# Optimization experiments

Hardware: AMD Instinct MI355X
Metric: run time of the kernel (lower is better)

The kernel has to match this reference:

```python
import jax, jax.numpy as jnp
import numpy as np

B, S, D_MODEL, H = 4, 1024, 1024, 16
HD = D_MODEL // H  # head_dim = 64


def setup_inputs() -> dict:
    key = jax.random.key(0)
    ks = jax.random.split(key, 12)
    sd = 1.0 / np.sqrt(D_MODEL)
    return {
        "x": jax.random.normal(ks[0], (B, S, D_MODEL), dtype=jnp.float32),
        "Wq": jax.random.normal(ks[1], (D_MODEL, D_MODEL), dtype=jnp.float32) * sd,
        "bq": jnp.zeros((D_MODEL,), dtype=jnp.float32),
        "Wk": jax.random.normal(ks[2], (D_MODEL, D_MODEL), dtype=jnp.float32) * sd,
        "bk": jnp.zeros((D_MODEL,), dtype=jnp.float32),
        "Wv": jax.random.normal(ks[3], (D_MODEL, D_MODEL), dtype=jnp.float32) * sd,
        "bv": jnp.zeros((D_MODEL,), dtype=jnp.float32),
        "W1": jax.random.normal(ks[4], (2 * D_MODEL, D_MODEL), dtype=jnp.float32) * sd,
        "b1": jnp.zeros((2 * D_MODEL,), dtype=jnp.float32),
        "W2": jax.random.normal(ks[5], (D_MODEL, 2 * D_MODEL), dtype=jnp.float32) * (1.0 / np.sqrt(2 * D_MODEL)),
        "b2": jnp.zeros((D_MODEL,), dtype=jnp.float32),
        "mask": jnp.ones((B, S, S), dtype=jnp.int32),
    }


def reference(x, Wq, bq, Wk, bk, Wv, bv, W1, b1, W2, b2, mask):
    # QKV projections (torch Linear: y = x @ W.T + b), split into heads -> [B,H,S,HD]
    def proj(W, b):
        return (x @ W.T + b).reshape(B, S, H, HD).transpose(0, 2, 1, 3)

    q = proj(Wq, bq)
    k = proj(Wk, bk)
    v = proj(Wv, bv)

    scores = jnp.einsum("bhqd,bhkd->bhqk", q, k) / jnp.sqrt(jnp.float32(HD))
    # mask [B,S,S] broadcast over heads (original does unsqueeze(1).repeat)
    scores = jnp.where(mask[:, None, :, :] == 0, jnp.float32(-1e8), scores)
    probs = jax.nn.softmax(scores, axis=-1)
    ctx = jnp.einsum("bhqk,bhkd->bhqd", probs, v)
    ctx = ctx.transpose(0, 2, 1, 3).reshape(B, S, D_MODEL)

    # out-projection MLP: Linear(d, 2d) -> ReLU -> Linear(2d, d)
    h = jax.nn.relu(ctx @ W1.T + b1)
    return h @ W2.T + b2
```

## Files before the change

kernel.cpp:

```cpp
#include <hip/hip_runtime.h>
#include <hip/hip_bf16.h>
#include <stdint.h>


#define B_ 4
#define S_ 1024
#define DM_ 1024
#define H_ 16
#define HD_ 64

typedef __attribute__((ext_vector_type(8))) short short8;
typedef __attribute__((ext_vector_type(4))) float f32x4;
typedef __attribute__((ext_vector_type(4))) unsigned short ushort4v;

#define GLB_AS(p) ((const __attribute__((address_space(1))) void*)(p))
#define LDS_AS(p) ((__attribute__((address_space(3))) void*)(p))

__device__ __forceinline__ void async_load16(const void* g, void* l) {
  __builtin_amdgcn_global_load_lds(GLB_AS(g), LDS_AS(l), 16, 0, 0);
}

__device__ __forceinline__ unsigned short f2bf(float x) {
  union { float f; unsigned int u; } v; v.f = x;
  unsigned int r = v.u + 0x7fffu + ((v.u >> 16) & 1u);
  return (unsigned short)(r >> 16);
}

#define QSCALE 0.18033688011112042f

struct ConvArgs {
  const float* src[6];
  unsigned short* dst[6];
  int n4[6];
};

__global__ void convert_bf16_kernel(ConvArgs a) {
  const int seg = blockIdx.y;
  const int n4 = a.n4[seg];
  const f32x4* __restrict__ src = (const f32x4*)a.src[seg];
  ushort4v* __restrict__ dst = (ushort4v*)a.dst[seg];
  for (int i = blockIdx.x * blockDim.x + threadIdx.x; i < n4;
       i += gridDim.x * blockDim.x) {
    f32x4 v = src[i];
    ushort4v o;
    o[0] = f2bf(v[0]); o[1] = f2bf(v[1]); o[2] = f2bf(v[2]); o[3] = f2bf(v[3]);
    dst[i] = o;
  }
}

__global__ void pack_mask_kernel(const int* __restrict__ mask,
                                 unsigned long long* __restrict__ bits,
                                 unsigned int* __restrict__ rowflag) {
  const int row = blockIdx.x * 4 + (threadIdx.x >> 6);
  const int lane = threadIdx.x & 63;
  const int* mr = mask + (size_t)row * S_;
  unsigned long long allf = ~0ull;
#pragma unroll
  for (int g = 0; g < 16; ++g) {
    int mv = mr[g * 64 + lane];
    unsigned long long bal = __ballot(mv != 0);
    if (lane == g) bits[(size_t)row * 16 + g] = bal;
    allf &= bal;
  }
  if (lane == 0) rowflag[row] = (allf == ~0ull) ? 1u : 0u;
}

__global__ void concat_bias_kernel(const float* __restrict__ bq,
                                   const float* __restrict__ bk,
                                   const float* __restrict__ bv,
                                   float* __restrict__ cb) {
  int i = blockIdx.x * 256 + threadIdx.x;
  const float* src = (i < 1024) ? bq : (i < 2048) ? bk : bv;
  cb[i] = src[i & 1023];
}

enum { EPI_QKV = 0, EPI_RELU_BF16 = 2, EPI_F32 = 3, EPI_PARTIAL = 4 };

template <int EPI>
__global__ __launch_bounds__(256, 3) void gemm_bt(
    const unsigned short* __restrict__ A, const unsigned short* __restrict__ Bt,
    const float* __restrict__ bias, void* __restrict__ Cp, int M, int N, int K,
    int Kld) {
  __shared__ unsigned short sA[128 * 32];
  __shared__ unsigned short sB[128 * 32];

  const int tid = threadIdx.x;
  const int lane = tid & 63;
  const int wave = tid >> 6;
  const int quad = lane >> 4;
  const int l15 = lane & 15;
  const int m0 = blockIdx.y * 128;
  const int n0 = blockIdx.x * 128;
  const int wm = (wave >> 1) * 64;
  const int wn = (wave & 1) * 64;
  const int kz = blockIdx.z * K;

  f32x4 acc[4][4];
#pragma unroll
  for (int i = 0; i < 4; ++i)
#pragma unroll
    for (int j = 0; j < 4; ++j) acc[i][j] = (f32x4){0.f, 0.f, 0.f, 0.f};

  const int srow = tid >> 2;
  const int scol = (tid & 3) * 8;
  const unsigned short* gA = A + (size_t)(m0 + srow) * Kld + kz + scol;
  const unsigned short* gB = Bt + (size_t)(n0 + srow) * Kld + kz + scol;
  unsigned short* lA = sA + tid * 8;
  unsigned short* lB = sB + tid * 8;

  for (int k0 = 0; k0 < K; k0 += 32) {
    __syncthreads();
    async_load16(gA + k0, lA);
    async_load16(gA + (size_t)64 * Kld + k0, lA + 64 * 32);
    async_load16(gB + k0, lB);
    async_load16(gB + (size_t)64 * Kld + k0, lB + 64 * 32);
    __syncthreads();

    short8 af[4], bfr[4];
#pragma unroll
    for (int t = 0; t < 4; ++t) {
      af[t] = *(const short8*)(sA + (wm + t * 16 + l15) * 32 + quad * 8);
      bfr[t] = *(const short8*)(sB + (wn + t * 16 + l15) * 32 + quad * 8);
    }
#pragma unroll
    for (int mt = 0; mt < 4; ++mt)
#pragma unroll
      for (int nt = 0; nt < 4; ++nt)
        acc[mt][nt] = __builtin_amdgcn_mfma_f32_16x16x32_bf16(
            af[mt], bfr[nt], acc[mt][nt], 0, 0, 0);
  }

#pragma unroll
  for (int nt = 0; nt < 4; ++nt) {
    const int col = n0 + wn + nt * 16 + l15;
    const float bv = (EPI == EPI_PARTIAL) ? 0.f : bias[col];
#pragma unroll
    for (int mt = 0; mt < 4; ++mt) {
#pragma unroll
      for (int r = 0; r < 4; ++r) {
        const int row = m0 + wm + mt * 16 + quad * 4 + r;
        float v = acc[mt][nt][r] + bv;
        if (EPI == EPI_F32) {
          ((float*)Cp)[(size_t)row * N + col] = v;
        } else if (EPI == EPI_PARTIAL) {
          ((float*)Cp)[(size_t)blockIdx.z * M * N + (size_t)row * N + col] = v;
        } else if (EPI == EPI_RELU_BF16) {
          ((unsigned short*)Cp)[(size_t)row * N + col] = f2bf(fmaxf(v, 0.f));
        } else {
          const int proj = col >> 10;
          const int c = col & 1023;
          const int hh = c >> 6, dd = c & 63;
          const int bb = row >> 10, ss = row & 1023;
          size_t off = (size_t)proj * (B_ * H_ * S_ * HD_) +
                       (size_t)(bb * 16 + hh) * (S_ * HD_);
          if (proj == 2)
            off += (size_t)dd * S_ + ss;
          else
            off += (size_t)ss * HD_ + dd;
          const float scl = (proj == 0) ? QSCALE : 1.0f;
          ((unsigned short*)Cp)[off] = f2bf(v * scl);
        }
      }
    }
  }
}

__global__ __launch_bounds__(256, 2) void flash_attn(
    const unsigned short* __restrict__ Q, const unsigned short* __restrict__ Kh,
    const unsigned short* __restrict__ Vt,
    const unsigned long long* __restrict__ mbits,
    const unsigned int* __restrict__ mrowflag,
    unsigned short* __restrict__ ctx) {
  __shared__ unsigned short sK[128 * 64];
  __shared__ unsigned short sV[64 * 128];
  __shared__ unsigned short spb[4][32 * 136];

  const int tid = threadIdx.x;
  const int wave = tid >> 6;
  const int lane = tid & 63;
  const int quad = lane >> 4;
  const int l15 = lane & 15;
  const int bh = blockIdx.x;
  const int b = bh >> 4;
  const int h = bh & 15;
  const int qbase = blockIdx.y * 128 + wave * 32;

  const unsigned short* Qb = Q + (size_t)bh * S_ * HD_;
  const unsigned short* Kb = Kh + (size_t)bh * S_ * HD_;
  const unsigned short* Vb = Vt + (size_t)bh * HD_ * S_;
  unsigned short* pbuf = spb[wave];

  bool mask_all_ones;
  {
    unsigned int f = mrowflag[b * S_ + qbase + (lane & 31)];
    mask_all_ones = (__ballot(f != 0) == ~0ull);
  }

  short8 qf[2][2];
#pragma unroll
  for (int u = 0; u < 2; ++u)
#pragma unroll
    for (int ks = 0; ks < 2; ++ks)
      qf[u][ks] = *(const short8*)(Qb + (size_t)(qbase + u * 16 + l15) * HD_ +
                                   ks * 32 + quad * 8);

  f32x4 o[2][4];
#pragma unroll
  for (int u = 0; u < 2; ++u)
#pragma unroll
    for (int i = 0; i < 4; ++i) o[u][i] = (f32x4){0.f, 0.f, 0.f, 0.f};
  float lsum[2][4] = {{0.f, 0.f, 0.f, 0.f}, {0.f, 0.f, 0.f, 0.f}};

  for (int kt = 0; kt < S_ / 128; ++kt) {
    const int kbase = kt * 128;

    __syncthreads();
#pragma unroll
    for (int st = 0; st < 4; ++st) {
      const int j = st * 256 + tid;
      const int r = j >> 3, c = j & 7;
      async_load16(Kb + (size_t)(kbase + r) * HD_ + ((c ^ (r & 7)) * 8),
                   sK + j * 8);
    }
#pragma unroll
    for (int st = 0; st < 4; ++st) {
      const int j = st * 256 + tid;
      const int d = j >> 4, c = j & 15;
      async_load16(Vb + (size_t)d * S_ + kbase + ((c ^ (d & 15)) * 8),
                   sV + j * 8);
    }
    __syncthreads();

    f32x4 s[2][8];
#pragma unroll
    for (int u = 0; u < 2; ++u)
#pragma unroll
      for (int i = 0; i < 8; ++i) s[u][i] = (f32x4){0.f, 0.f, 0.f, 0.f};
#pragma unroll
    for (int ks = 0; ks < 2; ++ks) {
      const int cg = ks * 4 + quad;
#pragma unroll
      for (int nt = 0; nt < 8; ++nt) {
        const int row = nt * 16 + l15;
        const short8 kf =
            *(const short8*)(sK + row * 64 + ((cg ^ (row & 7)) * 8));
        s[0][nt] = __builtin_amdgcn_mfma_f32_16x16x32_bf16(qf[0][ks], kf,
                                                           s[0][nt], 0, 0, 0);
        s[1][nt] = __builtin_amdgcn_mfma_f32_16x16x32_bf16(qf[1][ks], kf,
                                                           s[1][nt], 0, 0, 0);
      }
    }

    if (!mask_all_ones) {
#pragma unroll
      for (int u = 0; u < 2; ++u)
#pragma unroll
        for (int r = 0; r < 4; ++r) {
          const int q = qbase + u * 16 + quad * 4 + r;
          const unsigned long long* wp =
              mbits + ((size_t)(b * S_ + q)) * 16 + kt * 2;
          const unsigned long long w0 = wp[0], w1 = wp[1];
#pragma unroll
          for (int nt = 0; nt < 8; ++nt) {
            const unsigned long long w = (nt < 4) ? w0 : w1;
            const int bit = (nt * 16 + l15) & 63;
            if (!((w >> bit) & 1)) s[u][nt][r] = -1.0e8f;
          }
        }
    }

#pragma unroll
    for (int u = 0; u < 2; ++u)
#pragma unroll
      for (int nt = 0; nt < 8; ++nt)
#pragma unroll
        for (int r = 0; r < 4; ++r) {
          const float p = __builtin_amdgcn_exp2f(s[u][nt][r]);
          lsum[u][r] += p;
          pbuf[(u * 16 + quad * 4 + r) * 136 + nt * 16 + l15] = f2bf(p);
        }

#pragma unroll
    for (int ks2 = 0; ks2 < 4; ++ks2) {
      const short8 pf0 =
          *(const short8*)(pbuf + l15 * 136 + ks2 * 32 + quad * 8);
      const short8 pf1 =
          *(const short8*)(pbuf + (16 + l15) * 136 + ks2 * 32 + quad * 8);
      const int cg = ks2 * 4 + quad;
#pragma unroll
      for (int nt = 0; nt < 4; ++nt) {
        const int d = nt * 16 + l15;
        const short8 vf =
            *(const short8*)(sV + d * 128 + ((cg ^ (d & 15)) * 8));
        o[0][nt] = __builtin_amdgcn_mfma_f32_16x16x32_bf16(pf0, vf, o[0][nt], 0, 0, 0);
        o[1][nt] = __builtin_amdgcn_mfma_f32_16x16x32_bf16(pf1, vf, o[1][nt], 0, 0, 0);
      }
    }
  }

#pragma unroll
  for (int u = 0; u < 2; ++u)
#pragma unroll
    for (int r = 0; r < 4; ++r) {
      float lr = lsum[u][r];
      lr += __shfl_xor(lr, 1);
      lr += __shfl_xor(lr, 2);
      lr += __shfl_xor(lr, 4);
      lr += __shfl_xor(lr, 8);
      const float inv = 1.0f / lr;
#pragma unroll
      for (int nt = 0; nt < 4; ++nt)
        pbuf[(u * 16 + quad * 4 + r) * 68 + nt * 16 + l15] =
            f2bf(o[u][nt][r] * inv);
    }
#pragma unroll
  for (int i = 0; i < 4; ++i) {
    const int j = i * 64 + lane;
    const int r = j >> 3, c = j & 7;
    const short8 val = *(const short8*)(pbuf + r * 68 + c * 8);
    *(short8*)(ctx + ((size_t)b * S_ + qbase + r) * DM_ + h * HD_ + c * 8) = val;
  }
}

__global__ void reduce_ffn2_kernel(const float* __restrict__ part,
                                   const float* __restrict__ b2,
                                   float* __restrict__ out) {
  const int i = blockIdx.x * 256 + threadIdx.x;
  const f32x4 a = ((const f32x4*)part)[i];
  const f32x4 b = ((const f32x4*)part)[i + (B_ * S_ * DM_ / 4)];
  const f32x4 bb = ((const f32x4*)b2)[i & 255];
  ((f32x4*)out)[i] = a + b + bb;
}

extern "C" void kernel_launch(void* const* d_in, const int* in_sizes, int n_in,
                              void* d_out, int out_size, void* d_ws,
                              size_t ws_size, hipStream_t stream) {
  const float* x = (const float*)d_in[0];
  const float* Wq = (const float*)d_in[1];
  const float* bq = (const float*)d_in[2];
  const float* Wk = (const float*)d_in[3];
  const float* bk = (const float*)d_in[4];
  const float* Wv = (const float*)d_in[5];
  const float* bv = (const float*)d_in[6];
  const float* W1 = (const float*)d_in[7];
  const float* b1 = (const float*)d_in[8];
  const float* W2 = (const float*)d_in[9];
  const float* b2 = (const float*)d_in[10];
  const int* mask = (const int*)d_in[11];
  float* out = (float*)d_out;

  char* ws = (char*)d_ws;
  unsigned short* xb   = (unsigned short*)(ws + 0);
  unsigned short* wqkv = (unsigned short*)(ws + 8388608);
  unsigned short* w1b  = (unsigned short*)(ws + 14680064);
  unsigned short* w2b  = (unsigned short*)(ws + 18874368);
  unsigned short* QKVh = (unsigned short*)(ws + 23068672);
  unsigned short* ctxb = (unsigned short*)(ws + 48234496);
  unsigned short* hb   = (unsigned short*)(ws + 56623104);
  unsigned long long* mbits = (unsigned long long*)(ws + 73400320);
  unsigned int* mrowflag    = (unsigned int*)(ws + 73924608);
  float* cb                 = (float*)(ws + 73940992);
  float* part = (float*)(ws + 23068672);

  ConvArgs ca;
  ca.src[0] = x;  ca.dst[0] = xb;               ca.n4[0] = (B_ * S_ * DM_) / 4;
  ca.src[1] = Wq; ca.dst[1] = wqkv;             ca.n4[1] = (DM_ * DM_) / 4;
  ca.src[2] = Wk; ca.dst[2] = wqkv + DM_ * DM_; ca.n4[2] = (DM_ * DM_) / 4;
  ca.src[3] = Wv; ca.dst[3] = wqkv + 2 * DM_ * DM_; ca.n4[3] = (DM_ * DM_) / 4;
  ca.src[4] = W1; ca.dst[4] = w1b;              ca.n4[4] = (2 * DM_ * DM_) / 4;
  ca.src[5] = W2; ca.dst[5] = w2b;              ca.n4[5] = (2 * DM_ * DM_) / 4;
  convert_bf16_kernel<<<dim3(256, 6), 256, 0, stream>>>(ca);

  pack_mask_kernel<<<dim3((B_ * S_) / 4), 256, 0, stream>>>(mask, mbits, mrowflag);
  concat_bias_kernel<<<dim3(12), 256, 0, stream>>>(bq, bk, bv, cb);

  const int M = B_ * S_;
  gemm_bt<EPI_QKV><<<dim3(3 * DM_ / 128, M / 128), 256, 0, stream>>>(
      xb, wqkv, cb, QKVh, M, 3 * DM_, DM_, DM_);

  flash_attn<<<dim3(B_ * H_, S_ / 128), 256, 0, stream>>>(
      QKVh, QKVh + B_ * H_ * S_ * HD_, QKVh + 2 * B_ * H_ * S_ * HD_,
      mbits, mrowflag, ctxb);

  gemm_bt<EPI_RELU_BF16><<<dim3((2 * DM_) / 128, M / 128), 256, 0, stream>>>(
      ctxb, w1b, b1, hb, M, 2 * DM_, DM_, DM_);

  gemm_bt<EPI_PARTIAL><<<dim3(DM_ / 128, M / 128, 2), 256, 0, stream>>>(
      hb, w2b, b2, part, M, DM_, DM_, 2 * DM_);
  reduce_ffn2_kernel<<<dim3(M * DM_ / 4 / 256), 256, 0, stream>>>(part, b2, out);
}
```

Measured before the change: 258.7 us.

## Deepen GEMM K-tile to 64 with XOR swizzle; store QKV row-major and transpose V separately

The GEMM K tile doubles from 32 to 64 and the LDS layout gets an XOR swizzle, which halves the number of barrier pairs per K loop and should avoid LDS bank conflicts. The QKV GEMM now writes a plain row-major [M,3072] bf16 output instead of the scattered head-split and transposed-V stores, so its epilogue writes are coalesced. A new transpose_v kernel builds V^T (stored in the now-free xb region), and flash_attn reads Q and K with a 3072 row stride. The trade-offs are one more kernel launch, an extra pass over V, strided Q/K loads in attention, and more LDS per GEMM block, which may lower occupancy.

Result: faster. 246.1 us (-4.9%).

```diff
diff --git a/kernel.cpp b/kernel.cpp
--- a/kernel.cpp
+++ b/kernel.cpp
@@ -81,14 +81,15 @@
     const unsigned short* __restrict__ A, const unsigned short* __restrict__ Bt,
     const float* __restrict__ bias, void* __restrict__ Cp, int M, int N, int K,
     int Kld) {
-  __shared__ unsigned short sA[128 * 32];
-  __shared__ unsigned short sB[128 * 32];
+  __shared__ unsigned short sA[128 * 64];
+  __shared__ unsigned short sB[128 * 64];
 
   const int tid = threadIdx.x;
   const int lane = tid & 63;
   const int wave = tid >> 6;
   const int quad = lane >> 4;
   const int l15 = lane & 15;
+  const int swzb = l15 & 7;
   const int m0 = blockIdx.y * 128;
   const int n0 = blockIdx.x * 128;
   const int wm = (wave >> 1) * 64;
@@ -101,39 +102,45 @@
 #pragma unroll
     for (int j = 0; j < 4; ++j) acc[i][j] = (f32x4){0.f, 0.f, 0.f, 0.f};
 
-  const int srow = tid >> 2;
-  const int scol = (tid & 3) * 8;
+  const int srow = tid >> 3;
+  const int scol = ((tid & 7) ^ (srow & 7)) * 8;
   const unsigned short* gA = A + (size_t)(m0 + srow) * Kld + kz + scol;
   const unsigned short* gB = Bt + (size_t)(n0 + srow) * Kld + kz + scol;
   unsigned short* lA = sA + tid * 8;
   unsigned short* lB = sB + tid * 8;
 
-  for (int k0 = 0; k0 < K; k0 += 32) {
+  for (int k0 = 0; k0 < K; k0 += 64) {
     __syncthreads();
-    async_load16(gA + k0, lA);
-    async_load16(gA + (size_t)64 * Kld + k0, lA + 64 * 32);
-    async_load16(gB + k0, lB);
-    async_load16(gB + (size_t)64 * Kld + k0, lB + 64 * 32);
+#pragma unroll
+    for (int st = 0; st < 4; ++st) {
+      async_load16(gA + (size_t)(st * 32) * Kld + k0, lA + st * 2048);
+      async_load16(gB + (size_t)(st * 32) * Kld + k0, lB + st * 2048);
+    }
     __syncthreads();
 
-    short8 af[4], bfr[4];
-#pragma unroll
-    for (int t = 0; t < 4; ++t) {
-      af[t] = *(const short8*)(sA + (wm + t * 16 + l15) * 32 + quad * 8);
-      bfr[t] = *(const short8*)(sB + (wn + t * 16 + l15) * 32 + quad * 8);
-    }
-#pragma unroll
-    for (int mt = 0; mt < 4; ++mt)
-#pragma unroll
-      for (int nt = 0; nt < 4; ++nt)
-        acc[mt][nt] = __builtin_amdgcn_mfma_f32_16x16x32_bf16(
-            af[mt], bfr[nt], acc[mt][nt], 0, 0, 0);
+#pragma unroll
+    for (int ks = 0; ks < 2; ++ks) {
+      short8 af[4], bfr[4];
+#pragma unroll
+      for (int t = 0; t < 4; ++t) {
+        const int cg = ((ks * 4 + quad) ^ swzb) * 8;
+        af[t] = *(const short8*)(sA + (wm + t * 16 + l15) * 64 + cg);
+        bfr[t] = *(const short8*)(sB + (wn + t * 16 + l15) * 64 + cg);
+      }
+#pragma unroll
+      for (int mt = 0; mt < 4; ++mt)
+#pragma unroll
+        for (int nt = 0; nt < 4; ++nt)
+          acc[mt][nt] = __builtin_amdgcn_mfma_f32_16x16x32_bf16(
+              af[mt], bfr[nt], acc[mt][nt], 0, 0, 0);
+    }
   }
 
 #pragma unroll
   for (int nt = 0; nt < 4; ++nt) {
     const int col = n0 + wn + nt * 16 + l15;
     const float bv = (EPI == EPI_PARTIAL) ? 0.f : bias[col];
+    const float scl = (EPI == EPI_QKV && col < 1024) ? QSCALE : 1.0f;
 #pragma unroll
     for (int mt = 0; mt < 4; ++mt) {
 #pragma unroll
@@ -147,27 +154,45 @@
         } else if (EPI == EPI_RELU_BF16) {
           ((unsigned short*)Cp)[(size_t)row * N + col] = f2bf(fmaxf(v, 0.f));
         } else {
-          const int proj = col >> 10;
-          const int c = col & 1023;
-          const int hh = c >> 6, dd = c & 63;
-          const int bb = row >> 10, ss = row & 1023;
-          size_t off = (size_t)proj * (B_ * H_ * S_ * HD_) +
-                       (size_t)(bb * 16 + hh) * (S_ * HD_);
-          if (proj == 2)
-            off += (size_t)dd * S_ + ss;
-          else
-            off += (size_t)ss * HD_ + dd;
-          const float scl = (proj == 0) ? QSCALE : 1.0f;
-          ((unsigned short*)Cp)[off] = f2bf(v * scl);
+          ((unsigned short*)Cp)[(size_t)row * N + col] = f2bf(v * scl);
         }
       }
     }
   }
 }
 
+__global__ __launch_bounds__(256) void transpose_v(
+    const unsigned short* __restrict__ Cqkv, unsigned short* __restrict__ Vt) {
+  __shared__ unsigned short t[128 * 65];
+  const int bh = blockIdx.x;
+  const int stile = blockIdx.y;
+  const int b = bh >> 4, h = bh & 15;
+  const int tid = threadIdx.x;
+  const unsigned short* src =
+      Cqkv + ((size_t)(b * S_) + stile * 128) * 3072 + 2048 + h * 64;
+#pragma unroll
+  for (int ps = 0; ps < 4; ++ps) {
+    const int idx = ps * 256 + tid;
+    const int r = idx >> 3, c = idx & 7;
+    const short8 v = *(const short8*)(src + (size_t)r * 3072 + c * 8);
+#pragma unroll
+    for (int i = 0; i < 8; ++i) t[r * 65 + c * 8 + i] = (unsigned short)v[i];
+  }
+  __syncthreads();
+  unsigned short* dst = Vt + (size_t)bh * HD_ * S_ + stile * 128;
+#pragma unroll
+  for (int ps = 0; ps < 4; ++ps) {
+    const int idx = ps * 256 + tid;
+    const int d = idx >> 4, sc = idx & 15;
+    short8 v;
+#pragma unroll
+    for (int i = 0; i < 8; ++i) v[i] = (short)t[(sc * 8 + i) * 65 + d];
+    *(short8*)(dst + (size_t)d * S_ + sc * 8) = v;
+  }
+}
+
 __global__ __launch_bounds__(256, 2) void flash_attn(
-    const unsigned short* __restrict__ Q, const unsigned short* __restrict__ Kh,
-    const unsigned short* __restrict__ Vt,
+    const unsigned short* __restrict__ Cqkv, const unsigned short* __restrict__ Vt,
     const unsigned long long* __restrict__ mbits,
     const unsigned int* __restrict__ mrowflag,
     unsigned short* __restrict__ ctx) {
@@ -185,8 +210,8 @@
   const int h = bh & 15;
   const int qbase = blockIdx.y * 128 + wave * 32;
 
-  const unsigned short* Qb = Q + (size_t)bh * S_ * HD_;
-  const unsigned short* Kb = Kh + (size_t)bh * S_ * HD_;
+  const unsigned short* Qb = Cqkv + (size_t)(b * S_) * 3072 + h * HD_;
+  const unsigned short* Kb = Cqkv + (size_t)(b * S_) * 3072 + DM_ + h * HD_;
   const unsigned short* Vb = Vt + (size_t)bh * HD_ * S_;
   unsigned short* pbuf = spb[wave];
 
@@ -201,7 +226,7 @@
   for (int u = 0; u < 2; ++u)
 #pragma unroll
     for (int ks = 0; ks < 2; ++ks)
-      qf[u][ks] = *(const short8*)(Qb + (size_t)(qbase + u * 16 + l15) * HD_ +
+      qf[u][ks] = *(const short8*)(Qb + (size_t)(qbase + u * 16 + l15) * 3072 +
                                    ks * 32 + quad * 8);
 
   f32x4 o[2][4];
@@ -219,7 +244,7 @@
     for (int st = 0; st < 4; ++st) {
       const int j = st * 256 + tid;
       const int r = j >> 3, c = j & 7;
-      async_load16(Kb + (size_t)(kbase + r) * HD_ + ((c ^ (r & 7)) * 8),
+      async_load16(Kb + (size_t)(kbase + r) * 3072 + ((c ^ (r & 7)) * 8),
                    sK + j * 8);
     }
 #pragma unroll
@@ -351,10 +376,11 @@
 
   char* ws = (char*)d_ws;
   unsigned short* xb   = (unsigned short*)(ws + 0);
+  unsigned short* Vt   = (unsigned short*)(ws + 0);
   unsigned short* wqkv = (unsigned short*)(ws + 8388608);
   unsigned short* w1b  = (unsigned short*)(ws + 14680064);
   unsigned short* w2b  = (unsigned short*)(ws + 18874368);
-  unsigned short* QKVh = (unsigned short*)(ws + 23068672);
+  unsigned short* Cqkv = (unsigned short*)(ws + 23068672);
   unsigned short* ctxb = (unsigned short*)(ws + 48234496);
   unsigned short* hb   = (unsigned short*)(ws + 56623104);
   unsigned long long* mbits = (unsigned long long*)(ws + 73400320);
@@ -376,11 +402,12 @@
 
   const int M = B_ * S_;
   gemm_bt<EPI_QKV><<<dim3(3 * DM_ / 128, M / 128), 256, 0, stream>>>(
-      xb, wqkv, cb, QKVh, M, 3 * DM_, DM_, DM_);
+      xb, wqkv, cb, Cqkv, M, 3 * DM_, DM_, DM_);
+
+  transpose_v<<<dim3(B_ * H_, S_ / 128), 256, 0, stream>>>(Cqkv, Vt);
 
   flash_attn<<<dim3(B_ * H_, S_ / 128), 256, 0, stream>>>(
-      QKVh, QKVh + B_ * H_ * S_ * HD_, QKVh + 2 * B_ * H_ * S_ * HD_,
-      mbits, mrowflag, ctxb);
+      Cqkv, Vt, mbits, mrowflag, ctxb);
 
   gemm_bt<EPI_RELU_BF16><<<dim3((2 * DM_) / 128, M / 128), 256, 0, stream>>>(
       ctxb, w1b, b1, hb, M, 2 * DM_, DM_, DM_);
```
